# Optimization experiments

Measured on AMD Instinct MI355X. Metric: run time of the kernel, lower is better.

The kernel has to match this reference:

```python
import jax, jax.numpy as jnp
import numpy as np

N_NODES = 40962
LATENT_DIM = 512
N_EDGES = 655392
NUM_BLOCKS = 4
NUM_HEADS = 4
NUM_FREQ = 32
BASE_PERIOD = 16
NOISE_EMB_DIM = 16
EPS = 1e-5


def setup_inputs() -> dict:
    key = jax.random.key(0)
    ks = jax.random.split(key, 20)
    def w(k, shape, s=0.02):
        return jax.random.normal(k, shape, dtype=jnp.float32) * s
    D, B, C = LATENT_DIM, NUM_BLOCKS, NOISE_EMB_DIM
    z = lambda *s: jnp.zeros(s, jnp.float32)
    return {
        'latent_mesh_nodes': jax.random.normal(ks[0], (N_NODES, D), dtype=jnp.float32),
        'edge_index': jax.random.randint(ks[1], (2, N_EDGES), 0, N_NODES, dtype=jnp.int32),
        'noise_levels': jax.random.uniform(ks[2], (N_NODES, 1), dtype=jnp.float32),
        # Fourier embedding MLP (2F -> C -> C, SiLU)
        'f_w1': w(ks[3], (2 * NUM_FREQ, C)), 'f_b1': z(C),
        'f_w2': w(ks[4], (C, C)), 'f_b2': z(C),
        # per-block conditional LayerNorm 1 (FiLM)
        's1_w': w(ks[5], (B, C, D)), 's1_b': z(B, D),
        'b1_w': w(ks[6], (B, C, D)), 'b1_b': z(B, D),
        # per-block sparse MHA projections
        'wq': w(ks[7], (B, D, D)), 'bq': z(B, D),
        'wk': w(ks[8], (B, D, D)), 'bk': z(B, D),
        'wv': w(ks[9], (B, D, D)), 'bv': z(B, D),
        'wo': w(ks[10], (B, D, D)), 'bo': z(B, D),
        # per-block conditional LayerNorm 2 (FiLM)
        's2_w': w(ks[11], (B, C, D)), 's2_b': z(B, D),
        'b2_w': w(ks[12], (B, C, D)), 'b2_b': z(B, D),
        # per-block feed-forward MLP (D -> D -> D, ReLU)
        'm_w1': w(ks[13], (B, D, D)), 'm_b1': z(B, D),
        'm_w2': w(ks[14], (B, D, D)), 'm_b2': z(B, D),
    }


def _cond_layer_norm(x, cond, sw, sb, bw, bb):
    # LayerNorm without affine params, then FiLM from noise embedding.
    mu = jnp.mean(x, axis=-1, keepdims=True)
    var = jnp.var(x, axis=-1, keepdims=True)
    xn = (x - mu) * jax.lax.rsqrt(var + EPS)
    scale = cond @ sw + sb  # (N, D)
    bias = cond @ bw + bb
    return xn * (1.0 + scale) + bias


def _sparse_attention(x, src, dst, wq, bq, wk, bk, wv, bv, wo, bo):
    N, D = x.shape
    H, Dh = NUM_HEADS, D // NUM_HEADS
    q = ((x @ wq + bq)).reshape(N, H, Dh) * (Dh ** -0.5)
    k = (x @ wk + bk).reshape(N, H, Dh)
    v = (x @ wv + bv).reshape(N, H, Dh)
    # per-edge scores: row (query) = src, col (key) = dst, per head
    scores = jnp.einsum('ehd,ehd->eh', q[src], k[dst])  # (E, H)
    smax = jax.ops.segment_max(scores, src, num_segments=N)  # (N, H)
    ex = jnp.exp(scores - smax[src])
    denom = jax.ops.segment_sum(ex, src, num_segments=N)
    attn = ex / denom[src]  # row-wise sparse softmax
    out = jax.ops.segment_sum(attn[:, :, None] * v[dst], src, num_segments=N)
    return out.reshape(N, D) @ wo + bo


def _forward(x, edge_index, noise_levels, f_w1, f_b1, f_w2, f_b2,
             s1_w, s1_b, b1_w, b1_b, wq, bq, wk, bk, wv, bv, wo, bo,
             s2_w, s2_b, b2_w, b2_b, m_w1, m_b1, m_w2, m_b2):
    src, dst = edge_index[0], edge_index[1]
    # Fourier noise embedding
    freqs = jnp.arange(1, NUM_FREQ + 1, dtype=x.dtype) * (2.0 * np.pi / BASE_PERIOD)
    ph = noise_levels * freqs  # (N, F)
    emb = jnp.concatenate([jnp.sin(ph), jnp.cos(ph)], axis=-1)
    cond = jax.nn.silu(emb @ f_w1 + f_b1) @ f_w2 + f_b2  # (N, C)
    for i in range(NUM_BLOCKS):
        y = _cond_layer_norm(x, cond, s1_w[i], s1_b[i], b1_w[i], b1_b[i])
        y = _sparse_attention(y, src, dst, wq[i], bq[i], wk[i], bk[i],
                              wv[i], bv[i], wo[i], bo[i])
        x = x + y
        y = _cond_layer_norm(x, cond, s2_w[i], s2_b[i], b2_w[i], b2_b[i])
        y = jax.nn.relu(y @ m_w1[i] + m_b1[i]) @ m_w2[i] + m_b2[i]
        x = x + y
    return x


def reference(latent_mesh_nodes, edge_index, noise_levels, f_w1, f_b1, f_w2, f_b2,
              s1_w, s1_b, b1_w, b1_b, wq, bq, wk, bk, wv, bv, wo, bo,
              s2_w, s2_b, b2_w, b2_b, m_w1, m_b1, m_w2, m_b2):
    return _forward(latent_mesh_nodes, edge_index, noise_levels, f_w1, f_b1, f_w2, f_b2,
                    s1_w, s1_b, b1_w, b1_b, wq, bq, wk, bk, wv, bv, wo, bo,
                    s2_w, s2_b, b2_w, b2_b, m_w1, m_b1, m_w2, m_b2)
```

## Files before the change

### kernel.cpp

```cpp
#include <hip/hip_runtime.h>
#include <hip/hip_bf16.h>
#include <stdint.h>

#define N_NODES 40962
#define LATENT  512
#define N_EDGES 655392
#define NFREQ   32
#define NOISE_C 16

typedef unsigned short u16;
typedef unsigned char u8;
typedef __attribute__((ext_vector_type(8))) short short8;
typedef __attribute__((ext_vector_type(4))) float f32x4;
typedef __attribute__((ext_vector_type(2))) float f32x2;

__device__ __forceinline__ float bf2f(u16 u) {
  return __uint_as_float(((uint32_t)u) << 16);
}
__device__ __forceinline__ u16 f2bf(float f) {
  uint32_t u = __float_as_uint(f);
  u += 0x7fffu + ((u >> 16) & 1u);
  return (u16)(u >> 16);
}

__device__ __forceinline__ u8 f2fp8(float f) {
#if __has_builtin(__builtin_amdgcn_cvt_pk_fp8_f32)
  int pk = __builtin_amdgcn_cvt_pk_fp8_f32(f, f, 0, false);
  return (u8)(pk & 0xff);
#else
  uint32_t x = __float_as_uint(f);
  uint32_t s = (x >> 24) & 0x80;
  uint32_t y = x & 0x7fffffff;
  if (__uint_as_float(y) >= 448.f) return (u8)(s | 0x7e);
  y += 0xfffff + ((y >> 20) & 1);
  int e = (int)(y >> 23) - 127 + 7;
  uint32_t m = (y >> 20) & 7;
  if (e < 1) return (u8)s;
  if (e > 15 || (e == 15 && m == 7)) return (u8)(s | 0x7e);
  return (u8)(s | ((uint32_t)e << 3) | m);
#endif
}

__device__ __forceinline__ void fp8x4_to_f32(uint32_t w, float* o) {
#if __has_builtin(__builtin_amdgcn_cvt_pk_f32_fp8)
  f32x2 lo = __builtin_amdgcn_cvt_pk_f32_fp8(w, false);
  f32x2 hi = __builtin_amdgcn_cvt_pk_f32_fp8(w, true);
  o[0] = lo.x; o[1] = lo.y; o[2] = hi.x; o[3] = hi.y;
#else
  #pragma unroll
  for (int i = 0; i < 4; ++i) {
    uint32_t u = (w >> (8 * i)) & 0xff;
    uint32_t e = (u >> 3) & 15, m = u & 7, s = (u & 0x80) << 24;
    o[i] = (e == 0) ? __uint_as_float(s)
                    : __uint_as_float(s | ((e + 120) << 23) | (m << 20));
  }
#endif
}

__device__ __forceinline__ int xcd_remap(int id, int nwg) {
  int q = nwg >> 3, r = nwg & 7;
  int xc = id & 7, jj = id >> 3;
  return (xc < r ? xc * (q + 1) : r * (q + 1) + (xc - r) * q) + jj;
}

__global__ void cond_kernel(const float* __restrict__ noise,
                            const float* __restrict__ w1, const float* __restrict__ b1,
                            const float* __restrict__ w2, const float* __restrict__ b2,
                            float* __restrict__ cond)
{
  int n = blockIdx.x * blockDim.x + threadIdx.x;
  if (n >= N_NODES) return;
  float nv = noise[n];
  float emb[2 * NFREQ];
  #pragma unroll
  for (int f = 0; f < NFREQ; ++f) {
    float ph = nv * (0.39269908169872414f * (float)(f + 1));
    emb[f] = __sinf(ph);
    emb[NFREQ + f] = __cosf(ph);
  }
  float h[NOISE_C];
  #pragma unroll
  for (int c = 0; c < NOISE_C; ++c) {
    float a = b1[c];
    for (int j = 0; j < 2 * NFREQ; ++j) a = fmaf(emb[j], w1[j * NOISE_C + c], a);
    h[c] = a * (1.f / (1.f + __expf(-a)));
  }
  #pragma unroll
  for (int c2 = 0; c2 < NOISE_C; ++c2) {
    float a = b2[c2];
    #pragma unroll
    for (int c = 0; c < NOISE_C; ++c) a = fmaf(h[c], w2[c * NOISE_C + c2], a);
    cond[(size_t)n * NOISE_C + c2] = a;
  }
}

__global__ void conv_weights(const float* __restrict__ wq, const float* __restrict__ wk,
                             const float* __restrict__ wv, const float* __restrict__ wo,
                             const float* __restrict__ m1, const float* __restrict__ m2,
                             u16* __restrict__ out)
{
  __shared__ float tile[32][33];
  int z = blockIdx.z;
  int t6 = z >> 2;
  const float* W = (t6 == 0) ? wq : (t6 == 1) ? wk : (t6 == 2) ? wv :
                   (t6 == 3) ? wo : (t6 == 4) ? m1 : m2;
  W += (size_t)(z & 3) * 262144;
  u16* O = out + (size_t)((z & 3) * 6 + t6) * 262144;
  int tx = threadIdx.x, ty = threadIdx.y;
  int j0 = blockIdx.x * 32, k0 = blockIdx.y * 32;
  #pragma unroll
  for (int r = ty; r < 32; r += 8)
    tile[r][tx] = W[(size_t)(k0 + r) * 512 + j0 + tx];
  __syncthreads();
  #pragma unroll
  for (int r = ty; r < 32; r += 8)
    O[(size_t)(j0 + r) * 512 + k0 + tx] = f2bf(tile[tx][r]);
}

__global__ void pack_bias(const float* __restrict__ bq, const float* __restrict__ bk,
                          const float* __restrict__ bv, float* __restrict__ bqkv)
{
  int idx = blockIdx.x * 256 + threadIdx.x;
  if (idx >= 4 * 1536) return;
  int i = idx / 1536, c = idx % 1536;
  float v = (c < 512) ? bq[i * 512 + c] : (c < 1024) ? bk[i * 512 + c - 512]
                                                     : bv[i * 512 + c - 1024];
  bqkv[idx] = v;
}

__global__ void hist_kernel(const int* __restrict__ src, int* __restrict__ deg) {
  int e = blockIdx.x * 256 + threadIdx.x;
  if (e < N_EDGES) atomicAdd(&deg[src[e]], 1);
}

__global__ __launch_bounds__(1024) void scan_kernel(const int* __restrict__ deg,
                                                    int* __restrict__ row_start)
{
  __shared__ int sums[1024];
  int t = threadIdx.x;
  const int chunk = (N_NODES + 1023) / 1024;
  int lo = t * chunk, hi = lo + chunk;
  if (lo > N_NODES) lo = N_NODES;
  if (hi > N_NODES) hi = N_NODES;
  int s = 0;
  for (int i = lo; i < hi; ++i) s += deg[i];
  sums[t] = s;
  __syncthreads();
  for (int off = 1; off < 1024; off <<= 1) {
    int v = (t >= off) ? sums[t - off] : 0;
    __syncthreads();
    sums[t] += v;
    __syncthreads();
  }
  int base = (t > 0) ? sums[t - 1] : 0;
  for (int i = lo; i < hi; ++i) { row_start[i] = base; base += deg[i]; }
  if (t == 1023) row_start[N_NODES] = sums[1023];
}

__global__ void scatter_kernel(const int* __restrict__ src, const int* __restrict__ dst,
                               const int* __restrict__ row_start, int* __restrict__ cursor,
                               int* __restrict__ csr_dst)
{
  int e = blockIdx.x * 256 + threadIdx.x;
  if (e >= N_EDGES) return;
  int s = src[e];
  int p = atomicAdd(&cursor[s], 1);
  csr_dst[row_start[s] + p] = dst[e];
}

__global__ __launch_bounds__(256) void ln_film(
  const float* __restrict__ x, const float* __restrict__ cond,
  const float* __restrict__ sw, const float* __restrict__ sb,
  const float* __restrict__ bw, const float* __restrict__ bb,
  u16* __restrict__ yb)
{
  int n = blockIdx.x;
  int t = threadIdx.x;
  const float* xr = x + (size_t)n * 512;
  float v0 = xr[t], v1 = xr[t + 256];
  float s = v0 + v1, ss = v0 * v0 + v1 * v1;
  #pragma unroll
  for (int o = 32; o > 0; o >>= 1) { s += __shfl_down(s, o); ss += __shfl_down(ss, o); }
  __shared__ float red[8];
  __shared__ float cl[16];
  int wv_ = t >> 6, ln_ = t & 63;
  if (ln_ == 0) { red[wv_] = s; red[4 + wv_] = ss; }
  if (t < 16) cl[t] = cond[(size_t)n * 16 + t];
  __syncthreads();
  s  = red[0] + red[1] + red[2] + red[3];
  ss = red[4] + red[5] + red[6] + red[7];
  float mu = s * (1.f / 512.f);
  float rstd = rsqrtf(ss * (1.f / 512.f) - mu * mu + 1e-5f);
  #pragma unroll
  for (int k = 0; k < 2; ++k) {
    int d = t + k * 256;
    float sc = sb[d], bi = bb[d];
    #pragma unroll
    for (int c = 0; c < 16; ++c) {
      sc = fmaf(cl[c], sw[c * 512 + d], sc);
      bi = fmaf(cl[c], bw[c * 512 + d], bi);
    }
    float xv = k ? v1 : v0;
    yb[(size_t)n * 512 + d] = f2bf((xv - mu) * rstd * (1.f + sc) + bi);
  }
}

__global__ __launch_bounds__(512, 2) void gemm256_qkv(
  const u16* __restrict__ A, const u16* __restrict__ Bt,
  const float* __restrict__ bias, u8* __restrict__ Cq)
{
  constexpr int M = N_NODES;
  constexpr int NBX = 6;
  constexpr int NT = 8;
  __shared__ u16 As[2][256 * 64];
  __shared__ u16 Bs[2][256 * 64];
  int tid = threadIdx.x;
  int wid = tid >> 6, lane = tid & 63;
  int wm = wid >> 2, wn = wid & 3;
  int fm = lane & 15, fq = lane >> 4;
  int l3 = lane >> 3, l7 = lane & 7;
  int swz16 = (l7 ^ l3) * 8;

  int wg = xcd_remap(blockIdx.x, gridDim.x);
  int tn = (wg % NBX) * 256;
  int tm = (wg / NBX) * 256;

  f32x4 acc[8][4] = {};

  auto stage_half = [&](u16* ldsmat, const u16* __restrict__ G, int rowbase,
                        int h, int t, bool clampM) {
    #pragma unroll
    for (int rr = 0; rr < 2; ++rr) {
      int rowblk = h * 128 + (wid * 2 + rr) * 8;
      int grow = rowbase + rowblk + l3;
      if (clampM && grow > M - 1) grow = M - 1;
      const u16* src = G + (size_t)grow * 512 + t * 64 + swz16;
      u16* dstb = ldsmat + rowblk * 64;
      __builtin_amdgcn_global_load_lds(
        (const __attribute__((address_space(1))) void*)(uintptr_t)src,
        (__attribute__((address_space(3))) void*)(uintptr_t)dstb, 16, 0, 0);
    }
  };

  auto phase = [&](int d, int qm, int qn) {
    const u16* Ab = &As[d][0];
    const u16* Bb = &Bs[d][0];
    short8 a4[4][2], b2[2][2];
    #pragma unroll
    for (int i = 0; i < 4; ++i) {
      int ar = wm * 128 + qm * 64 + i * 16 + fm;
      #pragma unroll
      for (int ks = 0; ks < 2; ++ks)
        a4[i][ks] = *(const short8*)(Ab + ar * 64 + ((ks * 32 + fq * 8) ^ ((fm & 7) * 8)));
    }
    #pragma unroll
    for (int j = 0; j < 2; ++j) {
      int bc = wn * 64 + qn * 32 + j * 16 + fm;
      #pragma unroll
      for (int ks = 0; ks < 2; ++ks)
        b2[j][ks] = *(const short8*)(Bb + bc * 64 + ((ks * 32 + fq * 8) ^ ((fm & 7) * 8)));
    }
    __builtin_amdgcn_s_setprio(1);
    #pragma unroll
    for (int i = 0; i < 4; ++i)
      #pragma unroll
      for (int j = 0; j < 2; ++j)
        #pragma unroll
        for (int ks = 0; ks < 2; ++ks)
          acc[qm * 4 + i][qn * 2 + j] = __builtin_amdgcn_mfma_f32_16x16x32_bf16(
              a4[i][ks], b2[j][ks], acc[qm * 4 + i][qn * 2 + j], 0, 0, 0);
    __builtin_amdgcn_s_setprio(0);
    __builtin_amdgcn_s_barrier();
    __builtin_amdgcn_sched_barrier(0);
  };

  stage_half(As[0], A, tm, 0, 0, true);
  stage_half(As[0], A, tm, 1, 0, true);
  stage_half(Bs[0], Bt, tn, 0, 0, false);
  stage_half(Bs[0], Bt, tn, 1, 0, false);

  #pragma unroll 2
  for (int t = 0; t < NT; ++t) {
    int d = t & 1;
    if (t + 1 < NT) {
      stage_half(As[d ^ 1], A, tm, 0, t + 1, true);
      stage_half(Bs[d ^ 1], Bt, tn, 0, t + 1, false);
      asm volatile("s_waitcnt vmcnt(4)" ::: "memory");
    } else {
      asm volatile("s_waitcnt vmcnt(0)" ::: "memory");
    }
    __builtin_amdgcn_sched_barrier(0);
    __builtin_amdgcn_s_barrier();
    __builtin_amdgcn_sched_barrier(0);
    phase(d, 0, 0);
    phase(d, 1, 0);
    if (t + 1 < NT) {
      stage_half(As[d ^ 1], A, tm, 1, t + 1, true);
      stage_half(Bs[d ^ 1], Bt, tn, 1, t + 1, false);
    }
    phase(d, 0, 1);
    phase(d, 1, 1);
  }

  #pragma unroll
  for (int i = 0; i < 8; ++i) {
    int rowb = tm + wm * 128 + i * 16 + fq * 4;
    #pragma unroll
    for (int j = 0; j < 4; ++j) {
      int col = tn + wn * 64 + j * 16 + fm;
      float bvv = bias[col];
      #pragma unroll
      for (int r = 0; r < 4; ++r) {
        int gr = rowb + r;
        if (gr < M) {
          float v = acc[i][j][r] + bvv;
          u8* row_p = Cq + (size_t)gr * 2048;
          if (col < 512) *(u16*)(row_p + 2 * col) = f2bf(v);
          else           row_p[512 + col] = f2fp8(v);
        }
      }
    }
  }
}

template<int MODE, bool RELU, bool RES>
__global__ __launch_bounds__(256) void gemm_bt(
  const u16* __restrict__ A, const u16* __restrict__ Bt,
  const float* __restrict__ bias, const float* __restrict__ res,
  float* __restrict__ Cf, u16* __restrict__ Cb, int nbx)
{
  constexpr int M = N_NODES, K = 512;
  __shared__ u16 As[2 * 128 * 32];
  __shared__ u16 Bs[2 * 128 * 32];
  int tid = threadIdx.x;
  int wave = tid >> 6, lane = tid & 63;
  int wg = xcd_remap(blockIdx.x, gridDim.x);
  int tn = (wg % nbx) * 128, tm = (wg / nbx) * 128;
  f32x4 acc[4][4] = {};
  int wm = (wave & 1) * 64, wn = (wave >> 1) * 64;
  int fm = lane & 15, fq = lane >> 4;

  auto stage = [&](int buf, int k0) {
    #pragma unroll
    for (int rr = 0; rr < 2; ++rr) {
      int c = rr * 256 + tid;
      int row = c >> 2, cb = (c & 3) << 3;
      int gr = tm + row; if (gr > M - 1) gr = M - 1;
      __builtin_amdgcn_global_load_lds(
        (const __attribute__((address_space(1))) void*)(uintptr_t)(A + (size_t)gr * K + (k0 + cb)),
        (__attribute__((address_space(3))) void*)(uintptr_t)(As + buf * 4096 + (size_t)(rr * 256 + wave * 64) * 8),
        16, 0, 0);
      int brow = tn + row;
      __builtin_amdgcn_global_load_lds(
        (const __attribute__((address_space(1))) void*)(uintptr_t)(Bt + (size_t)brow * K + (k0 + cb)),
        (__attribute__((address_space(3))) void*)(uintptr_t)(Bs + buf * 4096 + (size_t)(rr * 256 + wave * 64) * 8),
        16, 0, 0);
    }
  };

  stage(0, 0);
  #pragma unroll 4
  for (int it = 0; it < K / 32; ++it) {
    int cur = it & 1;
    __syncthreads();
    if (it + 1 < K / 32) stage(cur ^ 1, (it + 1) * 32);
    const u16* Ab = As + cur * 4096;
    const u16* Bb = Bs + cur * 4096;
    short8 af[4], bf_[4];
    #pragma unroll
    for (int i = 0; i < 4; ++i) {
      af[i]  = *(const short8*)(Ab + (wm + i * 16 + fm) * 32 + fq * 8);
      bf_[i] = *(const short8*)(Bb + (wn + i * 16 + fm) * 32 + fq * 8);
    }
    #pragma unroll
    for (int mi = 0; mi < 4; ++mi)
      #pragma unroll
      for (int ni = 0; ni < 4; ++ni)
        acc[mi][ni] = __builtin_amdgcn_mfma_f32_16x16x32_bf16(af[mi], bf_[ni], acc[mi][ni], 0, 0, 0);
  }

  #pragma unroll
  for (int mi = 0; mi < 4; ++mi) {
    #pragma unroll
    for (int ni = 0; ni < 4; ++ni) {
      int col = tn + wn + ni * 16 + fm;
      float bvv = bias[col];
      int rowb = tm + wm + mi * 16 + fq * 4;
      #pragma unroll
      for (int r = 0; r < 4; ++r) {
        int gr = rowb + r;
        if (gr < M) {
          float v = acc[mi][ni][r] + bvv;
          if (RELU) v = fmaxf(v, 0.f);
          if (RES)  v += res[(size_t)gr * 512 + col];
          if (MODE == 0) Cf[(size_t)gr * 512 + col] = v;
          else           Cb[(size_t)gr * 512 + col] = f2bf(v);
        }
      }
    }
  }
}

__global__ __launch_bounds__(256) void attn_kernel(
  const u8* __restrict__ qkv,
  const int* __restrict__ row_start, const int* __restrict__ csr_dst,
  u16* __restrict__ ab)
{
  int wave = threadIdx.x >> 6, lane = threadIdx.x & 63;
  int n = blockIdx.x * 4 + wave;
  if (n >= N_NODES) return;
  float qf[8];
  {
    short8 q8 = *(const short8*)(qkv + (size_t)n * 2048 + lane * 16);
    #pragma unroll
    for (int j = 0; j < 8; ++j) qf[j] = bf2f((u16)q8[j]);
  }
  float m = -1e30f, l = 0.f;
  float acc[8];
  #pragma unroll
  for (int j = 0; j < 8; ++j) acc[j] = 0.f;
  int e0 = row_start[n], e1 = row_start[n + 1];
  int deg = e1 - e0;
  if (deg > 0) {
    int koff = 1024 + lane * 8, voff = 1536 + lane * 8;
    int d0 = csr_dst[e0];
    int d1 = (deg > 1) ? csr_dst[e0 + 1] : d0;
    uint2 ku0 = *(const uint2*)(qkv + (size_t)d0 * 2048 + koff);
    uint2 vu0 = *(const uint2*)(qkv + (size_t)d0 * 2048 + voff);
    uint2 ku1 = *(const uint2*)(qkv + (size_t)d1 * 2048 + koff);
    uint2 vu1 = *(const uint2*)(qkv + (size_t)d1 * 2048 + voff);
    for (int t = 0; t < deg; t += 2) {
      int p0 = e0 + t + 2, p1 = e0 + t + 3;
      int dn0 = (p0 < e1) ? csr_dst[p0] : d0;
      int dn1 = (p1 < e1) ? csr_dst[p1] : d0;
      uint2 kn0 = *(const uint2*)(qkv + (size_t)dn0 * 2048 + koff);
      uint2 vn0 = *(const uint2*)(qkv + (size_t)dn0 * 2048 + voff);
      uint2 kn1 = *(const uint2*)(qkv + (size_t)dn1 * 2048 + koff);
      uint2 vn1 = *(const uint2*)(qkv + (size_t)dn1 * 2048 + voff);
      float k0f[8], k1f[8];
      fp8x4_to_f32(ku0.x, k0f); fp8x4_to_f32(ku0.y, k0f + 4);
      fp8x4_to_f32(ku1.x, k1f); fp8x4_to_f32(ku1.y, k1f + 4);
      float s0 = 0.f, s1 = 0.f;
      #pragma unroll
      for (int j = 0; j < 8; ++j) { s0 = fmaf(qf[j], k0f[j], s0); s1 = fmaf(qf[j], k1f[j], s1); }
      s0 += __shfl_xor(s0, 1); s1 += __shfl_xor(s1, 1);
      s0 += __shfl_xor(s0, 2); s1 += __shfl_xor(s1, 2);
      s0 += __shfl_xor(s0, 4); s1 += __shfl_xor(s1, 4);
      s0 += __shfl_xor(s0, 8); s1 += __shfl_xor(s1, 8);
      s0 *= 0.088388347648318447f;
      s1 = (t + 1 < deg) ? s1 * 0.088388347648318447f : -1e30f;
      float mx = fmaxf(m, fmaxf(s0, s1));
      float al = __expf(m - mx);
      float pp0 = __expf(s0 - mx);
      float pp1 = __expf(s1 - mx);
      l = l * al + pp0 + pp1;
      float v0f[8], v1f[8];
      fp8x4_to_f32(vu0.x, v0f); fp8x4_to_f32(vu0.y, v0f + 4);
      fp8x4_to_f32(vu1.x, v1f); fp8x4_to_f32(vu1.y, v1f + 4);
      #pragma unroll
      for (int j = 0; j < 8; ++j)
        acc[j] = fmaf(acc[j], al, fmaf(pp0, v0f[j], pp1 * v1f[j]));
      m = mx;
      ku0 = kn0; vu0 = vn0; ku1 = kn1; vu1 = vn1;
    }
  }
  float rl = (l > 0.f) ? 1.f / l : 0.f;
  short8 o8;
  #pragma unroll
  for (int j = 0; j < 8; ++j) o8[j] = (short)f2bf(acc[j] * rl);
  *(short8*)(ab + (size_t)n * 512 + lane * 8) = o8;
}

extern "C" void kernel_launch(void* const* d_in, const int* in_sizes, int n_in,
                              void* d_out, int out_size, void* d_ws, size_t ws_size,
                              hipStream_t stream)
{
  const float* x0    = (const float*)d_in[0];
  const int*   edge  = (const int*)d_in[1];
  const float* noise = (const float*)d_in[2];
  const float* f_w1  = (const float*)d_in[3];
  const float* f_b1  = (const float*)d_in[4];
  const float* f_w2  = (const float*)d_in[5];
  const float* f_b2  = (const float*)d_in[6];
  const float* s1_w  = (const float*)d_in[7];
  const float* s1_b  = (const float*)d_in[8];
  const float* b1_w  = (const float*)d_in[9];
  const float* b1_b  = (const float*)d_in[10];
  const float* wq    = (const float*)d_in[11];
  const float* bq    = (const float*)d_in[12];
  const float* wk    = (const float*)d_in[13];
  const float* bk    = (const float*)d_in[14];
  const float* wv    = (const float*)d_in[15];
  const float* bv    = (const float*)d_in[16];
  const float* wo    = (const float*)d_in[17];
  const float* bo    = (const float*)d_in[18];
  const float* s2_w  = (const float*)d_in[19];
  const float* s2_b  = (const float*)d_in[20];
  const float* b2_w  = (const float*)d_in[21];
  const float* b2_b  = (const float*)d_in[22];
  const float* m_w1  = (const float*)d_in[23];
  const float* m_b1  = (const float*)d_in[24];
  const float* m_w2  = (const float*)d_in[25];
  const float* m_b2  = (const float*)d_in[26];
  float* xout = (float*)d_out;

  char* w = (char*)d_ws;
  auto alloc = [&](size_t bytes) -> char* {
    char* p = w; w += (bytes + 255) & ~(size_t)255; return p;
  };
  u16*  Wt     = (u16*)alloc(24ull * 512 * 512 * 2);
  float* cond  = (float*)alloc((size_t)N_NODES * 16 * 4);
  float* bqkv  = (float*)alloc(4 * 1536 * 4);
  u16*  ybf    = (u16*)alloc((size_t)N_NODES * 512 * 2);
  u16*  hbf    = (u16*)alloc((size_t)N_NODES * 512 * 2);
  u8*   qkvb   = (u8*)alloc((size_t)N_NODES * 2048);
  int*  deg    = (int*)alloc((size_t)N_NODES * 4);
  int*  cursor = (int*)alloc((size_t)N_NODES * 4);
  int*  rowst  = (int*)alloc((size_t)(N_NODES + 1) * 4);
  int*  csrd   = (int*)alloc((size_t)N_EDGES * 4);

  conv_weights<<<dim3(16, 16, 24), dim3(32, 8), 0, stream>>>(wq, wk, wv, wo, m_w1, m_w2, Wt);
  cond_kernel<<<(N_NODES + 255) / 256, 256, 0, stream>>>(noise, f_w1, f_b1, f_w2, f_b2, cond);
  pack_bias<<<(4 * 1536 + 255) / 256, 256, 0, stream>>>(bq, bk, bv, bqkv);
  hipMemsetAsync(deg, 0, (size_t)N_NODES * 4, stream);
  hipMemsetAsync(cursor, 0, (size_t)N_NODES * 4, stream);
  const int* src = edge;
  const int* dst = edge + N_EDGES;
  hist_kernel<<<(N_EDGES + 255) / 256, 256, 0, stream>>>(src, deg);
  scan_kernel<<<1, 1024, 0, stream>>>(deg, rowst);
  scatter_kernel<<<(N_EDGES + 255) / 256, 256, 0, stream>>>(src, dst, rowst, cursor, csrd);

  const int g_qkv = 6 * ((N_NODES + 255) / 256);
  const int g_512 = 4 * ((N_NODES + 127) / 128);
  const float* xin = x0;
  for (int i = 0; i < 4; ++i) {
    const u16* Wb = Wt + (size_t)i * 6 * 262144;
    ln_film<<<N_NODES, 256, 0, stream>>>(xin, cond, s1_w + i * 8192, s1_b + i * 512,
                                         b1_w + i * 8192, b1_b + i * 512, ybf);
    gemm256_qkv<<<g_qkv, 512, 0, stream>>>(ybf, Wb, bqkv + i * 1536, qkvb);
    attn_kernel<<<(N_NODES + 3) / 4, 256, 0, stream>>>(qkvb, rowst, csrd, ybf);
    gemm_bt<0, false, true><<<g_512, 256, 0, stream>>>(ybf, Wb + 3 * 262144,
                                                       bo + i * 512, xin, xout, nullptr, 4);
    ln_film<<<N_NODES, 256, 0, stream>>>(xout, cond, s2_w + i * 8192, s2_b + i * 512,
                                         b2_w + i * 8192, b2_b + i * 512, ybf);
    gemm_bt<1, true, false><<<g_512, 256, 0, stream>>>(ybf, Wb + 4 * 262144,
                                                       m_b1 + i * 512, nullptr, nullptr, hbf, 4);
    gemm_bt<0, false, true><<<g_512, 256, 0, stream>>>(hbf, Wb + 5 * 262144,
                                                       m_b2 + i * 512, xout, xout, nullptr, 4);
    xin = xout;
  }
}
```

Before: 3.058 ms.

## Process 32 nodes per LN-FiLM block with register-cached FiLM weights; reuse GEMM fragments

The LayerNorm+FiLM kernel now handles 32 nodes per block. The FiLM weight columns are held in registers and reused across all 32 rows, and the next row's x is prefetched while the current row is reduced. This removes the per-node reload of 64 KB of FiLM weights and most of the per-block launch overhead. In the QKV GEMM, the A and B fragment loads are split out and the phase order is changed so that A or B fragments already in registers are reused between consecutive MFMA phases, cutting LDS reads. The cost is higher register pressure in both kernels and a serialized per-row loop with a barrier on each row.

```diff
diff --git a/kernel.cpp b/kernel.cpp
--- a/kernel.cpp
+++ b/kernel.cpp
@@ -168,40 +168,69 @@
   csr_dst[row_start[s] + p] = dst[e];
 }
 
-__global__ __launch_bounds__(256) void ln_film(
+#define LN_NPB 32
+__global__ __launch_bounds__(256, 4) void ln_film(
   const float* __restrict__ x, const float* __restrict__ cond,
   const float* __restrict__ sw, const float* __restrict__ sb,
   const float* __restrict__ bw, const float* __restrict__ bb,
   u16* __restrict__ yb)
 {
-  int n = blockIdx.x;
   int t = threadIdx.x;
-  const float* xr = x + (size_t)n * 512;
-  float v0 = xr[t], v1 = xr[t + 256];
-  float s = v0 + v1, ss = v0 * v0 + v1 * v1;
-  #pragma unroll
-  for (int o = 32; o > 0; o >>= 1) { s += __shfl_down(s, o); ss += __shfl_down(ss, o); }
-  __shared__ float red[8];
-  __shared__ float cl[16];
+  int nbase = blockIdx.x * LN_NPB;
+  int nlocal = N_NODES - nbase; if (nlocal > LN_NPB) nlocal = LN_NPB;
+
+  float swr[16][2], bwr[16][2];
+  #pragma unroll
+  for (int c = 0; c < 16; ++c) {
+    swr[c][0] = sw[c * 512 + t];       swr[c][1] = sw[c * 512 + t + 256];
+    bwr[c][0] = bw[c * 512 + t];       bwr[c][1] = bw[c * 512 + t + 256];
+  }
+  float sb0 = sb[t], sb1 = sb[t + 256];
+  float bb0 = bb[t], bb1 = bb[t + 256];
+
+  __shared__ float cl[LN_NPB][16];
+  #pragma unroll
+  for (int r = 0; r < (LN_NPB * 16) / 256; ++r) {
+    int idx = r * 256 + t;
+    int nn = nbase + (idx >> 4);
+    cl[idx >> 4][idx & 15] = (nn < N_NODES) ? cond[(size_t)nn * 16 + (idx & 15)] : 0.f;
+  }
+
+  __shared__ float red[2][8];
   int wv_ = t >> 6, ln_ = t & 63;
-  if (ln_ == 0) { red[wv_] = s; red[4 + wv_] = ss; }
-  if (t < 16) cl[t] = cond[(size_t)n * 16 + t];
-  __syncthreads();
-  s  = red[0] + red[1] + red[2] + red[3];
-  ss = red[4] + red[5] + red[6] + red[7];
-  float mu = s * (1.f / 512.f);
-  float rstd = rsqrtf(ss * (1.f / 512.f) - mu * mu + 1e-5f);
-  #pragma unroll
-  for (int k = 0; k < 2; ++k) {
-    int d = t + k * 256;
-    float sc = sb[d], bi = bb[d];
+
+  float v0 = x[(size_t)nbase * 512 + t];
+  float v1 = x[(size_t)nbase * 512 + t + 256];
+  for (int i = 0; i < nlocal; ++i) {
+    float n0 = 0.f, n1 = 0.f;
+    if (i + 1 < nlocal) {
+      const float* xr = x + (size_t)(nbase + i + 1) * 512;
+      n0 = xr[t]; n1 = xr[t + 256];
+    }
+    float s = v0 + v1, ss = v0 * v0 + v1 * v1;
+    #pragma unroll
+    for (int o = 32; o > 0; o >>= 1) { s += __shfl_down(s, o); ss += __shfl_down(ss, o); }
+    if (ln_ == 0) { red[i & 1][wv_] = s; red[i & 1][4 + wv_] = ss; }
+    __syncthreads();
+    s  = red[i & 1][0] + red[i & 1][1] + red[i & 1][2] + red[i & 1][3];
+    ss = red[i & 1][4] + red[i & 1][5] + red[i & 1][6] + red[i & 1][7];
+    float mu = s * (1.f / 512.f);
+    float rstd = rsqrtf(ss * (1.f / 512.f) - mu * mu + 1e-5f);
+    float cc[16];
+    #pragma unroll
+    for (int c = 0; c < 16; ++c) cc[c] = cl[i][c];
+    float sc0 = sb0, bi0 = bb0, sc1 = sb1, bi1 = bb1;
     #pragma unroll
     for (int c = 0; c < 16; ++c) {
-      sc = fmaf(cl[c], sw[c * 512 + d], sc);
-      bi = fmaf(cl[c], bw[c * 512 + d], bi);
-    }
-    float xv = k ? v1 : v0;
-    yb[(size_t)n * 512 + d] = f2bf((xv - mu) * rstd * (1.f + sc) + bi);
+      sc0 = fmaf(cc[c], swr[c][0], sc0);
+      bi0 = fmaf(cc[c], bwr[c][0], bi0);
+      sc1 = fmaf(cc[c], swr[c][1], sc1);
+      bi1 = fmaf(cc[c], bwr[c][1], bi1);
+    }
+    size_t rowo = (size_t)(nbase + i) * 512;
+    yb[rowo + t]       = f2bf((v0 - mu) * rstd * (1.f + sc0) + bi0);
+    yb[rowo + t + 256] = f2bf((v1 - mu) * rstd * (1.f + sc1) + bi1);
+    v0 = n0; v1 = n1;
   }
 }
 
@@ -226,6 +255,8 @@
   int tm = (wg / NBX) * 256;
 
   f32x4 acc[8][4] = {};
+  short8 af[4][2];
+  short8 bfr[2][2];
 
   auto stage_half = [&](u16* ldsmat, const u16* __restrict__ G, int rowbase,
                         int h, int t, bool clampM) {
@@ -242,24 +273,27 @@
     }
   };
 
-  auto phase = [&](int d, int qm, int qn) {
+  auto load_a = [&](int d, int qm) {
     const u16* Ab = &As[d][0];
-    const u16* Bb = &Bs[d][0];
-    short8 a4[4][2], b2[2][2];
     #pragma unroll
     for (int i = 0; i < 4; ++i) {
       int ar = wm * 128 + qm * 64 + i * 16 + fm;
       #pragma unroll
       for (int ks = 0; ks < 2; ++ks)
-        a4[i][ks] = *(const short8*)(Ab + ar * 64 + ((ks * 32 + fq * 8) ^ ((fm & 7) * 8)));
-    }
+        af[i][ks] = *(const short8*)(Ab + ar * 64 + ((ks * 32 + fq * 8) ^ ((fm & 7) * 8)));
+    }
+  };
+  auto load_b = [&](int d, int qn) {
+    const u16* Bb = &Bs[d][0];
     #pragma unroll
     for (int j = 0; j < 2; ++j) {
       int bc = wn * 64 + qn * 32 + j * 16 + fm;
       #pragma unroll
       for (int ks = 0; ks < 2; ++ks)
-        b2[j][ks] = *(const short8*)(Bb + bc * 64 + ((ks * 32 + fq * 8) ^ ((fm & 7) * 8)));
-    }
+        bfr[j][ks] = *(const short8*)(Bb + bc * 64 + ((ks * 32 + fq * 8) ^ ((fm & 7) * 8)));
+    }
+  };
+  auto mma = [&](int qm, int qn) {
     __builtin_amdgcn_s_setprio(1);
     #pragma unroll
     for (int i = 0; i < 4; ++i)
@@ -268,7 +302,7 @@
         #pragma unroll
         for (int ks = 0; ks < 2; ++ks)
           acc[qm * 4 + i][qn * 2 + j] = __builtin_amdgcn_mfma_f32_16x16x32_bf16(
-              a4[i][ks], b2[j][ks], acc[qm * 4 + i][qn * 2 + j], 0, 0, 0);
+              af[i][ks], bfr[j][ks], acc[qm * 4 + i][qn * 2 + j], 0, 0, 0);
     __builtin_amdgcn_s_setprio(0);
     __builtin_amdgcn_s_barrier();
     __builtin_amdgcn_sched_barrier(0);
@@ -292,14 +326,14 @@
     __builtin_amdgcn_sched_barrier(0);
     __builtin_amdgcn_s_barrier();
     __builtin_amdgcn_sched_barrier(0);
-    phase(d, 0, 0);
-    phase(d, 1, 0);
+    load_a(d, 0); load_b(d, 0); mma(0, 0);
+    load_b(d, 1);               mma(0, 1);
     if (t + 1 < NT) {
       stage_half(As[d ^ 1], A, tm, 1, t + 1, true);
       stage_half(Bs[d ^ 1], Bt, tn, 1, t + 1, false);
     }
-    phase(d, 0, 1);
-    phase(d, 1, 1);
+    load_a(d, 1);               mma(1, 1);
+    load_b(d, 0);               mma(1, 0);
   }
 
   #pragma unroll
@@ -530,19 +564,20 @@
   scan_kernel<<<1, 1024, 0, stream>>>(deg, rowst);
   scatter_kernel<<<(N_EDGES + 255) / 256, 256, 0, stream>>>(src, dst, rowst, cursor, csrd);
 
+  const int g_ln  = (N_NODES + LN_NPB - 1) / LN_NPB;
   const int g_qkv = 6 * ((N_NODES + 255) / 256);
   const int g_512 = 4 * ((N_NODES + 127) / 128);
   const float* xin = x0;
   for (int i = 0; i < 4; ++i) {
     const u16* Wb = Wt + (size_t)i * 6 * 262144;
-    ln_film<<<N_NODES, 256, 0, stream>>>(xin, cond, s1_w + i * 8192, s1_b + i * 512,
-                                         b1_w + i * 8192, b1_b + i * 512, ybf);
+    ln_film<<<g_ln, 256, 0, stream>>>(xin, cond, s1_w + i * 8192, s1_b + i * 512,
+                                      b1_w + i * 8192, b1_b + i * 512, ybf);
     gemm256_qkv<<<g_qkv, 512, 0, stream>>>(ybf, Wb, bqkv + i * 1536, qkvb);
     attn_kernel<<<(N_NODES + 3) / 4, 256, 0, stream>>>(qkvb, rowst, csrd, ybf);
     gemm_bt<0, false, true><<<g_512, 256, 0, stream>>>(ybf, Wb + 3 * 262144,
                                                        bo + i * 512, xin, xout, nullptr, 4);
-    ln_film<<<N_NODES, 256, 0, stream>>>(xout, cond, s2_w + i * 8192, s2_b + i * 512,
-                                         b2_w + i * 8192, b2_b + i * 512, ybf);
+    ln_film<<<g_ln, 256, 0, stream>>>(xout, cond, s2_w + i * 8192, s2_b + i * 512,
+                                      b2_w + i * 8192, b2_b + i * 512, ybf);
     gemm_bt<1, true, false><<<g_512, 256, 0, stream>>>(ybf, Wb + 4 * 262144,
                                                        m_b1 + i * 512, nullptr, nullptr, hbf, 4);
     gemm_bt<0, false, true><<<g_512, 256, 0, stream>>>(hbf, Wb + 5 * 262144,
```

New measurement: 2.695 ms. 11.9% less time.
